# Kernel tuning notes

Measured on AMD Instinct MI355X. Metric: run time of the kernel, lower is better.

The kernel has to match this reference:

```python
import math
import jax, jax.numpy as jnp
import numpy as np

DIM = 1024
NUM_HEADS = 16
HEAD_DIM = DIM // NUM_HEADS


def rotate_half(x):
    x1, x2 = jnp.split(x, 2, axis=-1)
    return jnp.concatenate((-x2, x1), axis=-1)


def rope_cos_sin(seq_len, head_dim, dtype):
    # angles: (S, D/2); duplicated to (S, D) so it applies to full head_dim
    pos = jnp.arange(seq_len, dtype=dtype)[:, None]
    inv = jnp.exp(jnp.arange(0, head_dim, 2, dtype=dtype) * (-(math.log(10000.0) / head_dim)))
    angles = pos * inv[None, :]
    angles = jnp.concatenate((angles, angles), axis=-1)  # (S, D)
    return jnp.cos(angles), jnp.sin(angles)


def setup_inputs() -> dict:
    key = jax.random.key(0)
    ks = jax.random.split(key, 5)
    B, S, C = 8, 1024, DIM
    scale = 1.0 / math.sqrt(C)
    return {
        "x": jax.random.normal(ks[0], (B, S, C), dtype=jnp.float32),
        "W_qkv": jax.random.normal(ks[1], (C, 3 * C), dtype=jnp.float32) * scale,
        "b_qkv": jax.random.normal(ks[2], (3 * C,), dtype=jnp.float32) * 0.02,
        "W_proj": jax.random.normal(ks[3], (C, C), dtype=jnp.float32) * scale,
        "b_proj": jax.random.normal(ks[4], (C,), dtype=jnp.float32) * 0.02,
    }


def reference(x, W_qkv, b_qkv, W_proj, b_proj):
    B, S, C = x.shape
    H, D = NUM_HEADS, C // NUM_HEADS
    scale = D ** -0.5

    qkv = x @ W_qkv + b_qkv                       # (B, S, 3C)
    qkv = qkv.reshape(B, S, 3, H, D).transpose(2, 0, 3, 1, 4)  # (3, B, H, S, D)
    q, k, v = qkv[0], qkv[1], qkv[2]

    cos, sin = rope_cos_sin(S, D, x.dtype)        # (S, D) each, broadcast over B,H
    q = q * cos + rotate_half(q) * sin
    k = k * cos + rotate_half(k) * sin

    attn = jnp.einsum("bhqd,bhkd->bhqk", q, k) * scale
    attn = jax.nn.softmax(attn, axis=-1)
    out = jnp.einsum("bhqk,bhkd->bhqd", attn, v)  # (B, H, S, D)
    out = out.transpose(0, 2, 1, 3).reshape(B, S, C)
    return out @ W_proj + b_proj
```

## Files before the change

### kernel.cpp

```cpp
#include <hip/hip_runtime.h>
#include <hip/hip_fp16.h>
#include <math.h>


typedef _Float16 half_t;
typedef _Float16 half8 __attribute__((ext_vector_type(8)));
typedef _Float16 half4v __attribute__((ext_vector_type(4)));
typedef float f32x4 __attribute__((ext_vector_type(4)));

#define MFMA16(a, b, c) __builtin_amdgcn_mfma_f32_16x16x32_f16(a, b, c, 0, 0, 0)

__device__ __forceinline__ void gload_lds16(const half_t* g, half_t* lds) {
  __builtin_amdgcn_global_load_lds(
      (const __attribute__((address_space(1))) void*)g,
      (__attribute__((address_space(3))) void*)lds, 16, 0, 0);
}

__global__ __launch_bounds__(256) void k_cvt(const float* __restrict__ in,
                                             half_t* __restrict__ out, int n4) {
  int i = blockIdx.x * blockDim.x + threadIdx.x;
  if (i >= n4) return;
  float4 v = ((const float4*)in)[i];
  half4v h;
  h.x = (half_t)v.x; h.y = (half_t)v.y; h.z = (half_t)v.z; h.w = (half_t)v.w;
  ((half4v*)out)[i] = h;
}

__global__ __launch_bounds__(256) void k_cvt_t(const float* __restrict__ in,
                                               half_t* __restrict__ out,
                                               int rows, int cols) {
  __shared__ half_t tile[32][33];
  int c0 = blockIdx.x * 32, r0 = blockIdx.y * 32;
  int tx = threadIdx.x & 31, g = threadIdx.x >> 5;
#pragma unroll
  for (int i = 0; i < 4; i++) {
    int r = g * 4 + i;
    tile[r][tx] = (half_t)in[(size_t)(r0 + r) * cols + c0 + tx];
  }
  __syncthreads();
#pragma unroll
  for (int i = 0; i < 4; i++) {
    int cc = g * 4 + i;
    out[(size_t)(c0 + cc) * rows + r0 + tx] = tile[tx][cc];
  }
}

__global__ __launch_bounds__(256) void k_rope_tab(float2* __restrict__ tab) {
  int idx = blockIdx.x * 256 + threadIdx.x;
  int s = idx >> 5, jj = idx & 31;
  float inv = expf(-0.28782313662425572f * (float)jj);
  float ang = (float)s * inv;
  float sn, cs;
  sincosf(ang, &sn, &cs);
  tab[idx] = make_float2(cs, sn);
}

template <int MODE>
__global__ __launch_bounds__(256) void k_gemm(
    const half_t* __restrict__ A, const half_t* __restrict__ Bt,
    const float* __restrict__ bias, const float2* __restrict__ rope,
    half_t* __restrict__ Qo, half_t* __restrict__ Ko, half_t* __restrict__ Vo,
    float* __restrict__ Fo) {
  __shared__ alignas(16) half_t smem[17408];
  half_t* As = smem;
  half_t* Bs = smem + 8192;
  const int t = threadIdx.x;
  const int lane = t & 63, w = t >> 6;
  const int quad = lane >> 4, cl = lane & 15;
  const int m0 = blockIdx.y * 128, n0 = blockIdx.x * 128;
  const int wm = (w >> 1) * 64, wn = (w & 1) * 64;

  f32x4 acc[4][4] = {};

  for (int kt = 0; kt < 1024; kt += 64) {
    __syncthreads();
#pragma unroll
    for (int cc = 0; cc < 4; cc++) {
      int lg = (w * 4 + cc) * 64 + lane;
      int row = lg >> 3;
      int gs = (lg & 7) ^ (row & 7);
      gload_lds16(A + (size_t)(m0 + row) * 1024 + kt + gs * 8,
                  As + (w * 4 + cc) * 512);
      gload_lds16(Bt + (size_t)(n0 + row) * 1024 + kt + gs * 8,
                  Bs + (w * 4 + cc) * 512);
    }
    __syncthreads();
#pragma unroll
    for (int ks = 0; ks < 2; ks++) {
      half8 af[4], bf[4];
#pragma unroll
      for (int i = 0; i < 4; i++) {
        int mr = wm + i * 16 + cl;
        af[i] = *(const half8*)(As + mr * 64 + (((ks * 4 + quad) ^ (mr & 7)) * 8));
        int nr = wn + i * 16 + cl;
        bf[i] = *(const half8*)(Bs + nr * 64 + (((ks * 4 + quad) ^ (nr & 7)) * 8));
      }
#pragma unroll
      for (int i = 0; i < 4; i++)
#pragma unroll
        for (int j = 0; j < 4; j++) acc[i][j] = MFMA16(af[i], bf[j], acc[i][j]);
    }
  }

  if (MODE == 0) {
    const int which = n0 >> 10;
    if (which == 2) {
      __syncthreads();
      half_t* T = smem;
#pragma unroll
      for (int i = 0; i < 4; i++)
#pragma unroll
        for (int j = 0; j < 4; j++)
#pragma unroll
          for (int r = 0; r < 4; r++) {
            int n = n0 + wn + j * 16 + cl;
            T[(wn + j * 16 + cl) * 136 + (wm + i * 16 + quad * 4 + r)] =
                (half_t)(acc[i][j][r] + bias[n]);
          }
      __syncthreads();
      const int b = m0 >> 10, sbase = m0 & 1023;
#pragma unroll
      for (int u = 0; u < 8; u++) {
        int ci = u * 256 + t;
        int drow = ci >> 4, scol = (ci & 15) * 8;
        half8 val = *(const half8*)(T + drow * 136 + scol);
        int n = n0 + drow;
        int hh = (n >> 6) & 15, d = n & 63;
        *(half8*)(Vo + ((size_t)((b * 16 + hh) * 64 + d)) * 1024 + sbase + scol) = val;
      }
    } else {
#pragma unroll
      for (int i = 0; i < 4; i++)
#pragma unroll
        for (int r = 0; r < 4; r++) {
          int gm = m0 + wm + i * 16 + quad * 4 + r;
          int b = gm >> 10, s = gm & 1023;
#pragma unroll
          for (int j = 0; j < 4; j++) {
            int n = n0 + wn + j * 16 + cl;
            int d = n & 63, hh = (n >> 6) & 15;
            float v = acc[i][j][r] + bias[n];
            float pr = acc[i][j ^ 2][r] + bias[n ^ 32];
            float2 tr = rope[(s << 5) | (d & 31)];
            float rv = (d < 32) ? (v * tr.x - pr * tr.y) : (v * tr.x + pr * tr.y);
            size_t adr = ((size_t)((b * 16 + hh) * 1024 + s)) * 64 + d;
            if (which == 0)
              Qo[adr] = (half_t)(rv * 0.125f);
            else
              Ko[adr] = (half_t)rv;
          }
        }
    }
  } else {
#pragma unroll
    for (int i = 0; i < 4; i++)
#pragma unroll
      for (int r = 0; r < 4; r++) {
        int gm = m0 + wm + i * 16 + quad * 4 + r;
#pragma unroll
        for (int j = 0; j < 4; j++) {
          int n = n0 + wn + j * 16 + cl;
          Fo[(size_t)gm * 1024 + n] = acc[i][j][r] + bias[n];
        }
      }
  }
}

__global__ __launch_bounds__(256) void k_attn(const half_t* __restrict__ Qg_,
                                              const half_t* __restrict__ Kg_,
                                              const half_t* __restrict__ Vg_,
                                              half_t* __restrict__ Og) {
  __shared__ alignas(16) half_t Qs[8192];
  __shared__ alignas(16) half_t Ks[4096];
  __shared__ alignas(16) half_t Vs[4096];
  __shared__ alignas(16) half_t Ps[128 * 72];
  __shared__ float ilbuf[128];
  const int t = threadIdx.x, lane = t & 63, w = t >> 6;
  const int quad = lane >> 4, cl = lane & 15;
  const int bh = blockIdx.x, q0 = blockIdx.y * 128;
  const half_t* Qg = Qg_ + (size_t)bh * 65536;
  const half_t* Kg = Kg_ + (size_t)bh * 65536;
  const half_t* Vg = Vg_ + (size_t)bh * 65536;

#pragma unroll
  for (int cc = 0; cc < 4; cc++) {
    int lg = (w * 4 + cc) * 64 + lane;
    int row = lg >> 3;
    int gs = (lg & 7) ^ (row & 7);
    gload_lds16(Qg + (size_t)(q0 + row) * 64 + gs * 8, Qs + (w * 4 + cc) * 512);
  }
  __syncthreads();

  half8 qf[2][2];
#pragma unroll
  for (int ks = 0; ks < 2; ks++)
#pragma unroll
    for (int j = 0; j < 2; j++) {
      int qr = w * 32 + j * 16 + cl;
      qf[ks][j] = *(const half8*)(Qs + qr * 64 + (((ks * 4 + quad) ^ (qr & 7)) * 8));
    }

  f32x4 oacc[2][4] = {};
  float lsum[2] = {0.f, 0.f};

  for (int kt = 0; kt < 1024; kt += 64) {
    __syncthreads();
#pragma unroll
    for (int cc = 0; cc < 2; cc++) {
      int lg = (w * 2 + cc) * 64 + lane;
      int row = lg >> 3;
      int gs = (lg & 7) ^ (row & 7);
      gload_lds16(Kg + (size_t)(kt + row) * 64 + gs * 8, Ks + (w * 2 + cc) * 512);
      gload_lds16(Vg + (size_t)row * 1024 + kt + gs * 8, Vs + (w * 2 + cc) * 512);
    }
    __syncthreads();

    f32x4 sacc[4][2] = {};
#pragma unroll
    for (int ks = 0; ks < 2; ks++) {
      half8 kf[4];
#pragma unroll
      for (int i = 0; i < 4; i++) {
        int kr = i * 16 + cl;
        kf[i] = *(const half8*)(Ks + kr * 64 + (((ks * 4 + quad) ^ (kr & 7)) * 8));
      }
#pragma unroll
      for (int i = 0; i < 4; i++)
#pragma unroll
        for (int j = 0; j < 2; j++)
          sacc[i][j] = MFMA16(kf[i], qf[ks][j], sacc[i][j]);
    }

#pragma unroll
    for (int i = 0; i < 4; i++)
#pragma unroll
      for (int j = 0; j < 2; j++) {
        float p0 = __expf(sacc[i][j][0] - 8.f);
        float p1 = __expf(sacc[i][j][1] - 8.f);
        float p2 = __expf(sacc[i][j][2] - 8.f);
        float p3 = __expf(sacc[i][j][3] - 8.f);
        lsum[j] += (p0 + p1) + (p2 + p3);
        half4v pk;
        pk.x = (half_t)p0; pk.y = (half_t)p1; pk.z = (half_t)p2; pk.w = (half_t)p3;
        *(half4v*)(Ps + (w * 32 + j * 16 + cl) * 72 + i * 16 + quad * 4) = pk;
      }

#pragma unroll
    for (int ks = 0; ks < 2; ks++) {
      half8 pf[2], vf[4];
#pragma unroll
      for (int i = 0; i < 2; i++)
        pf[i] = *(const half8*)(Ps + (w * 32 + i * 16 + cl) * 72 + ks * 32 + quad * 8);
#pragma unroll
      for (int j = 0; j < 4; j++) {
        int dr = j * 16 + cl;
        vf[j] = *(const half8*)(Vs + dr * 64 + (((ks * 4 + quad) ^ (dr & 7)) * 8));
      }
#pragma unroll
      for (int i = 0; i < 2; i++)
#pragma unroll
        for (int j = 0; j < 4; j++) oacc[i][j] = MFMA16(pf[i], vf[j], oacc[i][j]);
    }
  }

#pragma unroll
  for (int j = 0; j < 2; j++) {
    float l = lsum[j];
    l += __shfl_xor(l, 16);
    l += __shfl_xor(l, 32);
    if (quad == 0) ilbuf[w * 32 + j * 16 + cl] = 1.f / l;
  }

  const int b = bh >> 4, hh = bh & 15;
#pragma unroll
  for (int i = 0; i < 2; i++)
#pragma unroll
    for (int r = 0; r < 4; r++) {
      float sc = ilbuf[w * 32 + i * 16 + quad * 4 + r];
      int srow = q0 + w * 32 + i * 16 + quad * 4 + r;
#pragma unroll
      for (int j = 0; j < 4; j++) {
        int d = j * 16 + cl;
        Og[((size_t)(b * 1024 + srow)) * 1024 + hh * 64 + d] =
            (half_t)(oacc[i][j][r] * sc);
      }
    }
}

extern "C" void kernel_launch(void* const* d_in, const int* in_sizes, int n_in,
                              void* d_out, int out_size, void* d_ws,
                              size_t ws_size, hipStream_t stream) {
  (void)in_sizes; (void)n_in; (void)out_size; (void)ws_size;
  const float* x = (const float*)d_in[0];
  const float* Wqkv = (const float*)d_in[1];
  const float* bqkv = (const float*)d_in[2];
  const float* Wproj = (const float*)d_in[3];
  const float* bproj = (const float*)d_in[4];
  float* out = (float*)d_out;

  half_t* ws = (half_t*)d_ws;
  half_t* x16 = ws;
  half_t* WqkvT = ws + 8388608;
  half_t* WprojT = ws + 11534336;
  half_t* Q16 = ws + 12582912;
  half_t* K16 = ws + 20971520;
  half_t* V16 = ws + 29360128;
  float2* rope = (float2*)(ws + 37748736);
  half_t* O16 = x16;

  k_cvt<<<8192, 256, 0, stream>>>(x, x16, 2097152);
  k_cvt_t<<<dim3(96, 32), 256, 0, stream>>>(Wqkv, WqkvT, 1024, 3072);
  k_cvt_t<<<dim3(32, 32), 256, 0, stream>>>(Wproj, WprojT, 1024, 1024);
  k_rope_tab<<<128, 256, 0, stream>>>(rope);
  k_gemm<0><<<dim3(24, 64), 256, 0, stream>>>(x16, WqkvT, bqkv, rope, Q16, K16,
                                              V16, nullptr);
  k_attn<<<dim3(128, 8), 256, 0, stream>>>(Q16, K16, V16, O16);
  k_gemm<1><<<dim3(8, 64), 256, 0, stream>>>(O16, WprojT, bproj, nullptr,
                                             nullptr, nullptr, nullptr, out);
}
```

Measured before the change: 252.6 us.

## Fuse prep kernels into one launch and stage Q/K epilogue through LDS

Merges the four preprocessing kernels (x conversion, two weight transposes, rope table) into a single launch that dispatches on block index, removing three kernel launch gaps. The Q/K epilogue of the QKV GEMM now writes rotated values into shared memory first, then emits 16-byte vector stores per head row. The old path issued scattered 2-byte stores. This adds two barriers and LDS traffic in exchange for coalesced global writes.

```diff
diff --git a/kernel.cpp b/kernel.cpp
--- a/kernel.cpp
+++ b/kernel.cpp
@@ -16,21 +16,11 @@
       (__attribute__((address_space(3))) void*)lds, 16, 0, 0);
 }
 
-__global__ __launch_bounds__(256) void k_cvt(const float* __restrict__ in,
-                                             half_t* __restrict__ out, int n4) {
-  int i = blockIdx.x * blockDim.x + threadIdx.x;
-  if (i >= n4) return;
-  float4 v = ((const float4*)in)[i];
-  half4v h;
-  h.x = (half_t)v.x; h.y = (half_t)v.y; h.z = (half_t)v.z; h.w = (half_t)v.w;
-  ((half4v*)out)[i] = h;
-}
-
-__global__ __launch_bounds__(256) void k_cvt_t(const float* __restrict__ in,
+__device__ __forceinline__ void prep_transpose(const float* __restrict__ in,
                                                half_t* __restrict__ out,
-                                               int rows, int cols) {
-  __shared__ half_t tile[32][33];
-  int c0 = blockIdx.x * 32, r0 = blockIdx.y * 32;
+                                               int rows, int cols, int bx,
+                                               int by, half_t (*tile)[33]) {
+  int c0 = bx * 32, r0 = by * 32;
   int tx = threadIdx.x & 31, g = threadIdx.x >> 5;
 #pragma unroll
   for (int i = 0; i < 4; i++) {
@@ -45,14 +35,34 @@
   }
 }
 
-__global__ __launch_bounds__(256) void k_rope_tab(float2* __restrict__ tab) {
-  int idx = blockIdx.x * 256 + threadIdx.x;
-  int s = idx >> 5, jj = idx & 31;
-  float inv = expf(-0.28782313662425572f * (float)jj);
-  float ang = (float)s * inv;
-  float sn, cs;
-  sincosf(ang, &sn, &cs);
-  tab[idx] = make_float2(cs, sn);
+__global__ __launch_bounds__(256) void k_prep(
+    const float* __restrict__ x, half_t* __restrict__ x16,
+    const float* __restrict__ Wqkv, half_t* __restrict__ WqkvT,
+    const float* __restrict__ Wproj, half_t* __restrict__ WprojT,
+    float2* __restrict__ rope) {
+  __shared__ half_t tile[32][33];
+  int bid = blockIdx.x;
+  if (bid < 8192) {
+    int i = bid * 256 + threadIdx.x;
+    float4 v = ((const float4*)x)[i];
+    half4v h;
+    h.x = (half_t)v.x; h.y = (half_t)v.y; h.z = (half_t)v.z; h.w = (half_t)v.w;
+    ((half4v*)x16)[i] = h;
+  } else if (bid < 11264) {
+    int idx = bid - 8192;
+    prep_transpose(Wqkv, WqkvT, 1024, 3072, idx % 96, idx / 96, tile);
+  } else if (bid < 12288) {
+    int idx = bid - 11264;
+    prep_transpose(Wproj, WprojT, 1024, 1024, idx & 31, idx >> 5, tile);
+  } else {
+    int idx = (bid - 12288) * 256 + threadIdx.x;
+    int s = idx >> 5, jj = idx & 31;
+    float inv = expf(-0.28782313662425572f * (float)jj);
+    float ang = (float)s * inv;
+    float sn, cs;
+    sincosf(ang, &sn, &cs);
+    rope[idx] = make_float2(cs, sn);
+  }
 }
 
 template <int MODE>
@@ -129,27 +139,40 @@
         *(half8*)(Vo + ((size_t)((b * 16 + hh) * 64 + d)) * 1024 + sbase + scol) = val;
       }
     } else {
+      __syncthreads();
+      half_t* T = smem;
+      const float qsc = (which == 0) ? 0.125f : 1.0f;
 #pragma unroll
       for (int i = 0; i < 4; i++)
 #pragma unroll
         for (int r = 0; r < 4; r++) {
-          int gm = m0 + wm + i * 16 + quad * 4 + r;
-          int b = gm >> 10, s = gm & 1023;
+          int ml = wm + i * 16 + quad * 4 + r;
+          int s = (m0 + ml) & 1023;
 #pragma unroll
           for (int j = 0; j < 4; j++) {
-            int n = n0 + wn + j * 16 + cl;
-            int d = n & 63, hh = (n >> 6) & 15;
+            int nl = wn + j * 16 + cl;
+            int n = n0 + nl;
+            int d = n & 63;
             float v = acc[i][j][r] + bias[n];
             float pr = acc[i][j ^ 2][r] + bias[n ^ 32];
             float2 tr = rope[(s << 5) | (d & 31)];
             float rv = (d < 32) ? (v * tr.x - pr * tr.y) : (v * tr.x + pr * tr.y);
-            size_t adr = ((size_t)((b * 16 + hh) * 1024 + s)) * 64 + d;
-            if (which == 0)
-              Qo[adr] = (half_t)(rv * 0.125f);
-            else
-              Ko[adr] = (half_t)rv;
+            T[ml * 136 + nl] = (half_t)(rv * qsc);
           }
         }
+      __syncthreads();
+      half_t* dst = (which == 0) ? Qo : Ko;
+      const int b = m0 >> 10;
+#pragma unroll
+      for (int u = 0; u < 8; u++) {
+        int ci = u * 256 + t;
+        int mrow = ci >> 4, ch = ci & 15;
+        half8 val = *(const half8*)(T + mrow * 136 + ch * 8);
+        int s = (m0 + mrow) & 1023;
+        int n = n0 + ch * 8;
+        int hh = (n >> 6) & 15, d = n & 63;
+        *(half8*)(dst + ((size_t)((b * 16 + hh) * 1024 + s)) * 64 + d) = val;
+      }
     }
   } else {
 #pragma unroll
@@ -308,10 +331,7 @@
   float2* rope = (float2*)(ws + 37748736);
   half_t* O16 = x16;
 
-  k_cvt<<<8192, 256, 0, stream>>>(x, x16, 2097152);
-  k_cvt_t<<<dim3(96, 32), 256, 0, stream>>>(Wqkv, WqkvT, 1024, 3072);
-  k_cvt_t<<<dim3(32, 32), 256, 0, stream>>>(Wproj, WprojT, 1024, 1024);
-  k_rope_tab<<<128, 256, 0, stream>>>(rope);
+  k_prep<<<12416, 256, 0, stream>>>(x, x16, Wqkv, WqkvT, Wproj, WprojT, rope);
   k_gemm<0><<<dim3(24, 64), 256, 0, stream>>>(x16, WqkvT, bqkv, rope, Q16, K16,
                                               V16, nullptr);
   k_attn<<<dim3(128, 8), 256, 0, stream>>>(Q16, K16, V16, O16);
```

Result: no change. 251.6 us (-0.4%).
